# Performance work log

Measured on AMD Instinct MI355X. Metric: run time of the kernel, lower is better.

Reference implementation:

```python
import jax, jax.numpy as jnp
import numpy as np

T_ROIS = 200                       # TRAIN_ROIS_PER_IMAGE
POS_MAX = int(200 * 0.33)          # 66 max positives
R_RATIO = 1.0 / 0.33               # negative:positive ratio constant
MASK_SIZE = 28
BBOX_STD = np.array([0.1, 0.1, 0.2, 0.2], dtype=np.float32)


def _pairwise_iou(b1, b2):
    # b1 [N,4], b2 [G,4] -> [N,G]
    y1 = jnp.maximum(b1[:, None, 0], b2[None, :, 0])
    x1 = jnp.maximum(b1[:, None, 1], b2[None, :, 1])
    y2 = jnp.minimum(b1[:, None, 2], b2[None, :, 2])
    x2 = jnp.minimum(b1[:, None, 3], b2[None, :, 3])
    inter = jnp.maximum(x2 - x1, 0.0) * jnp.maximum(y2 - y1, 0.0)
    a1 = (b1[:, 2] - b1[:, 0]) * (b1[:, 3] - b1[:, 1])
    a2 = (b2[:, 2] - b2[:, 0]) * (b2[:, 3] - b2[:, 1])
    union = a1[:, None] + a2[None, :] - inter
    return jnp.where(union > 0, inter / jnp.where(union > 0, union, 1.0), 0.0)


def _box_refinement(box, gt):
    h = box[:, 2] - box[:, 0]
    w = box[:, 3] - box[:, 1]
    cy = box[:, 0] + 0.5 * h
    cx = box[:, 1] + 0.5 * w
    gh = gt[:, 2] - gt[:, 0]
    gw = gt[:, 3] - gt[:, 1]
    gcy = gt[:, 0] + 0.5 * gh
    gcx = gt[:, 1] + 0.5 * gw
    return jnp.stack([(gcy - cy) / h, (gcx - cx) / w,
                      jnp.log(gh / h), jnp.log(gw / w)], axis=1)


def _crop_and_resize(images, boxes, size):
    # TF tf.image.crop_and_resize (bilinear, extrapolation 0), images [K,H,W], boxes [K,4]
    K, H, W = images.shape
    y1, x1, y2, x2 = boxes[:, 0], boxes[:, 1], boxes[:, 2], boxes[:, 3]
    i = jnp.arange(size, dtype=images.dtype)
    ys = y1[:, None] * (H - 1) + i[None, :] * ((y2 - y1) * (H - 1) / (size - 1))[:, None]  # [K,S]
    xs = x1[:, None] * (W - 1) + i[None, :] * ((x2 - x1) * (W - 1) / (size - 1))[:, None]
    y0 = jnp.floor(ys)
    x0 = jnp.floor(xs)
    wy = (ys - y0)[:, :, None]   # [K,S,1]
    wx = (xs - x0)[:, None, :]   # [K,1,S]
    y0i = jnp.clip(y0, 0, H - 1).astype(jnp.int32)
    y1i = jnp.clip(y0 + 1, 0, H - 1).astype(jnp.int32)
    x0i = jnp.clip(x0, 0, W - 1).astype(jnp.int32)
    x1i = jnp.clip(x0 + 1, 0, W - 1).astype(jnp.int32)
    kk = jnp.arange(K)[:, None, None]
    v00 = images[kk, y0i[:, :, None], x0i[:, None, :]]
    v01 = images[kk, y0i[:, :, None], x1i[:, None, :]]
    v10 = images[kk, y1i[:, :, None], x0i[:, None, :]]
    v11 = images[kk, y1i[:, :, None], x1i[:, None, :]]
    val = (v00 * (1 - wx) + v01 * wx) * (1 - wy) + (v10 * (1 - wx) + v11 * wx) * wy
    ok = ((ys >= 0) & (ys <= H - 1))[:, :, None] & ((xs >= 0) & (xs <= W - 1))[:, None, :]
    return jnp.where(ok, val, 0.0)


def _detection_targets(proposals, gt_class_ids, gt_boxes, gt_masks):
    # proposals [N,4] f32, gt_class_ids [G] int32, gt_boxes [G,4] f32, gt_masks [H,W,G] bool
    valid_prop = jnp.sum(jnp.abs(proposals), axis=1) > 0          # trim_zeros (as mask)
    valid_gt = jnp.sum(jnp.abs(gt_boxes), axis=1) > 0
    is_crowd = valid_gt & (gt_class_ids < 0)
    is_fg = valid_gt & (gt_class_ids > 0)
    iou = _pairwise_iou(proposals, gt_boxes)                       # [N,G]
    iou = jnp.where(valid_prop[:, None], iou, 0.0)
    crowd_max = jnp.max(jnp.where(is_crowd[None, :], iou, 0.0), axis=1)
    no_crowd = crowd_max < 1e-3
    roi_iou_max = jnp.max(jnp.where(is_fg[None, :], iou, 0.0), axis=1)
    pos_bool = (roi_iou_max >= 0.5) & valid_prop
    neg_bool = (roi_iou_max < 0.5) & no_crowd & valid_prop
    num_pos = jnp.minimum(jnp.sum(pos_bool), POS_MAX)
    num_neg_want = jnp.floor(R_RATIO * num_pos.astype(jnp.float32)).astype(jnp.int32) - num_pos
    num_neg = jnp.clip(jnp.minimum(num_neg_want, jnp.sum(neg_bool)), 0, T_ROIS - num_pos)
    # deterministic subsample: lowest-index positives/negatives first (stable argsort)
    pos_order = jnp.argsort(jnp.logical_not(pos_bool))
    neg_order = jnp.argsort(jnp.logical_not(neg_bool))
    j = jnp.arange(T_ROIS)
    is_p = j < num_pos
    is_n = (j >= num_pos) & (j < num_pos + num_neg)
    sel = jnp.where(is_p, pos_order[j], neg_order[jnp.maximum(j - num_pos, 0)])
    keep = (is_p | is_n).astype(proposals.dtype)
    rois = proposals[sel] * keep[:, None]                          # zero-padded tail
    assign = jnp.argmax(jnp.where(is_fg[None, :], iou, -1.0)[sel], axis=1)
    class_ids = jnp.where(is_p, gt_class_ids[assign], 0)
    dummy = jnp.array([0.0, 0.0, 1.0, 1.0], dtype=proposals.dtype)  # safe box for padded rows
    p_roi = jnp.where(is_p[:, None], rois, dummy)
    p_gt = jnp.where(is_p[:, None], gt_boxes[assign], dummy)
    deltas = _box_refinement(p_roi, p_gt) / jnp.asarray(BBOX_STD)
    deltas = deltas * is_p[:, None]
    # mask targets: only first POS_MAX slots can be positive
    masks_t = jnp.transpose(gt_masks.astype(proposals.dtype), (2, 0, 1))   # [G,H,W]
    roi_m = masks_t[assign[:POS_MAX]]                              # [66,H,W]
    m = _crop_and_resize(roi_m, p_roi[:POS_MAX], MASK_SIZE)
    m = jnp.round(m) * is_p[:POS_MAX, None, None]
    masks = jnp.pad(m, ((0, T_ROIS - POS_MAX), (0, 0), (0, 0)))
    return rois, class_ids, deltas, masks


def _rand_boxes(k, shape):
    yx1 = jax.random.uniform(k, shape + (2,)) * 0.7
    hw = jax.random.uniform(jax.random.fold_in(k, 1), shape + (2,)) * 0.28 + 0.02
    return jnp.stack([yx1[..., 0], yx1[..., 1],
                      yx1[..., 0] + hw[..., 0], yx1[..., 1] + hw[..., 1]], axis=-1)


def setup_inputs() -> dict:
    key = jax.random.key(0)
    ks = jax.random.split(key, 6)
    B, N, G, H, W = 2, 2000, 100, 512, 512
    proposals = _rand_boxes(ks[0], (B, N))
    proposals = proposals * (jnp.arange(N) < int(N * 0.9))[None, :, None]  # zero-padded tail
    gt_boxes = _rand_boxes(ks[1], (B, G))
    gt_valid = jnp.arange(G) < 80
    gt_boxes = gt_boxes * gt_valid[None, :, None]
    cls = jax.random.randint(ks[2], (B, G), 1, 81).astype(jnp.int32)
    crowd = jax.random.uniform(ks[3], (B, G)) < 0.05
    cls = jnp.where(crowd, -cls, cls)
    cls = jnp.where(gt_valid[None, :], cls, 0)
    gt_masks = jax.random.randint(ks[4], (B, H, W, G), 0, 2).astype(bool)
    return {"proposals": proposals, "gt_class_ids": cls,
            "gt_boxes": gt_boxes, "gt_masks": gt_masks}


def reference(proposals, gt_class_ids, gt_boxes, gt_masks):
    return jax.vmap(_detection_targets)(proposals, gt_class_ids, gt_boxes, gt_masks)
```

## Files before the change

kernel.cpp:

```cpp
#include <hip/hip_runtime.h>
#include <math.h>

#define NPROP 2000
#define NGT   100
#define HH    512
#define WW    512
#define TR    200
#define PMAX  66
#define MS    28
#define FLAGS_OFF 4096

__global__ __launch_bounds__(256) void k_flags(
    const float* __restrict__ props,
    const int*   __restrict__ gcls,
    const float* __restrict__ gbox,
    int* __restrict__ wsi)
{
    const int b = blockIdx.y;
    const int i = blockIdx.x * 256 + threadIdx.x;
    const float* P  = props + (size_t)b * NPROP * 4;
    const float* GB = gbox  + (size_t)b * NGT * 4;
    const int*   GC = gcls  + (size_t)b * NGT;

    __shared__ float s_gb[NGT][4];
    __shared__ float s_garea[NGT];
    __shared__ unsigned char s_fg[NGT], s_crowd[NGT];

    if (threadIdx.x < NGT) {
        int t = threadIdx.x;
        float g0 = GB[t*4+0], g1 = GB[t*4+1], g2 = GB[t*4+2], g3 = GB[t*4+3];
        s_gb[t][0]=g0; s_gb[t][1]=g1; s_gb[t][2]=g2; s_gb[t][3]=g3;
        bool vg = (fabsf(g0)+fabsf(g1)+fabsf(g2)+fabsf(g3)) > 0.0f;
        int c = GC[t];
        s_fg[t]    = (unsigned char)(vg && (c > 0));
        s_crowd[t] = (unsigned char)(vg && (c < 0));
        s_garea[t] = __fmul_rn(__fsub_rn(g2,g0), __fsub_rn(g3,g1));
    }
    __syncthreads();

    if (i >= NPROP) return;
    float p0=P[i*4+0], p1=P[i*4+1], p2=P[i*4+2], p3=P[i*4+3];
    bool vp = (fabsf(p0)+fabsf(p1)+fabsf(p2)+fabsf(p3)) > 0.0f;
    float a1 = __fmul_rn(__fsub_rn(p2,p0), __fsub_rn(p3,p1));
    float crowd_max = 0.0f, fgmax = 0.0f;
    float best = -INFINITY; int arg = 0;
    for (int g = 0; g < NGT; ++g) {
        float y1 = fmaxf(p0, s_gb[g][0]);
        float x1 = fmaxf(p1, s_gb[g][1]);
        float y2 = fminf(p2, s_gb[g][2]);
        float x2 = fminf(p3, s_gb[g][3]);
        float inter = __fmul_rn(fmaxf(__fsub_rn(x2,x1), 0.0f),
                                fmaxf(__fsub_rn(y2,y1), 0.0f));
        float un = __fsub_rn(__fadd_rn(a1, s_garea[g]), inter);
        float iou = (un > 0.0f) ? __fdiv_rn(inter, un) : 0.0f;
        if (!vp) iou = 0.0f;
        if (s_crowd[g]) crowd_max = fmaxf(crowd_max, iou);
        float v;
        if (s_fg[g]) { fgmax = fmaxf(fgmax, iou); v = iou; }
        else         { v = -1.0f; }
        if (v > best) { best = v; arg = g; }
    }
    int pos = (int)((fgmax >= 0.5f) && vp);
    int neg = (int)((fgmax < 0.5f) && (crowd_max < 0.001f) && vp);
    wsi[FLAGS_OFF + b*NPROP + i] = pos | (neg << 1) | (arg << 2);
}

__global__ __launch_bounds__(512) void k_pick(
    const float* __restrict__ props,
    const int*   __restrict__ gcls,
    const float* __restrict__ gbox,
    float* __restrict__ out,
    int* __restrict__ wsi)
{
    const int b = blockIdx.x;
    const int t = threadIdx.x;
    const float* P  = props + (size_t)b * NPROP * 4;
    const float* GB = gbox  + (size_t)b * NGT * 4;
    const int*   GC = gcls  + (size_t)b * NGT;
    const int*   F  = wsi + FLAGS_OFF + b * NPROP;

    __shared__ int s_selp[PMAX], s_seln[TR], s_selpg[PMAX];
    __shared__ int s_wp[8], s_wn[8];
    __shared__ int s_totp, s_totn, s_np, s_nn;

    int t4 = t * 4;
    int fl[4]; int cp = 0, cn = 0;
    #pragma unroll
    for (int e = 0; e < 4; ++e) {
        int i = t4 + e;
        fl[e] = (i < NPROP) ? F[i] : 0;
        cp += (fl[e] & 1); cn += ((fl[e] >> 1) & 1);
    }
    int ip = cp, inn = cn;
    int lane = t & 63;
    #pragma unroll
    for (int d = 1; d < 64; d <<= 1) {
        int vp2 = __shfl_up(ip, d);
        int vn2 = __shfl_up(inn, d);
        if (lane >= d) { ip += vp2; inn += vn2; }
    }
    if (lane == 63) { s_wp[t >> 6] = ip; s_wn[t >> 6] = inn; }
    __syncthreads();
    if (t == 0) {
        int ap = 0, an = 0;
        for (int w = 0; w < 8; ++w) {
            int tp = s_wp[w]; s_wp[w] = ap; ap += tp;
            int tn = s_wn[w]; s_wn[w] = an; an += tn;
        }
        s_totp = ap; s_totn = an;
    }
    __syncthreads();
    int ep = s_wp[t >> 6] + ip - cp;
    int en = s_wn[t >> 6] + inn - cn;
    #pragma unroll
    for (int e = 0; e < 4; ++e) {
        if (fl[e] & 1) { if (ep < PMAX) { s_selp[ep] = t4 + e; s_selpg[ep] = (fl[e] >> 2) & 127; } ep++; }
        if ((fl[e] >> 1) & 1) { if (en < TR) s_seln[en] = t4 + e; en++; }
    }
    __syncthreads();

    if (t == 0) {
        int np = min(s_totp, PMAX);
        const float R = (float)(1.0 / 0.33);
        int want = (int)floorf(__fmul_rn(R, (float)np)) - np;
        int nn = min(want, s_totn);
        nn = min(nn, TR - np);
        nn = max(nn, 0);
        s_np = np; s_nn = nn;
        wsi[b] = np;
    }
    __syncthreads();

    if (t < TR) {
        const int j = t;
        const int np = s_np, nn = s_nn;
        const bool isp  = j < np;
        const bool kept = j < np + nn;
        float r0=0, r1=0, r2=0, r3=0, cid=0, d0=0, d1=0, d2=0, d3=0;
        if (kept) {
            int sel = isp ? s_selp[j] : s_seln[j - np];
            r0 = P[sel*4+0]; r1 = P[sel*4+1]; r2 = P[sel*4+2]; r3 = P[sel*4+3];
            if (isp) {
                int g = s_selpg[j];
                cid = (float)GC[g];
                float gb0 = GB[g*4+0], gb1 = GB[g*4+1], gb2 = GB[g*4+2], gb3 = GB[g*4+3];
                float h  = __fsub_rn(r2, r0), w = __fsub_rn(r3, r1);
                float cy = __fadd_rn(r0, __fmul_rn(0.5f, h));
                float cx = __fadd_rn(r1, __fmul_rn(0.5f, w));
                float gh  = __fsub_rn(gb2, gb0);
                float gw  = __fsub_rn(gb3, gb1);
                float gcy = __fadd_rn(gb0, __fmul_rn(0.5f, gh));
                float gcx = __fadd_rn(gb1, __fmul_rn(0.5f, gw));
                d0 = __fdiv_rn(__fdiv_rn(__fsub_rn(gcy, cy), h), 0.1f);
                d1 = __fdiv_rn(__fdiv_rn(__fsub_rn(gcx, cx), w), 0.1f);
                d2 = __fdiv_rn(logf(__fdiv_rn(gh, h)), 0.2f);
                d3 = __fdiv_rn(logf(__fdiv_rn(gw, w)), 0.2f);
                if (j < PMAX) {
                    wsi[2 + b*PMAX + j] = g;
                    float* wsf = (float*)(wsi + 2 + 2*PMAX);
                    wsf[(b*PMAX + j)*4 + 0] = r0;
                    wsf[(b*PMAX + j)*4 + 1] = r1;
                    wsf[(b*PMAX + j)*4 + 2] = r2;
                    wsf[(b*PMAX + j)*4 + 3] = r3;
                }
            }
        }
        out[(size_t)b*TR*4 + j*4 + 0] = r0;
        out[(size_t)b*TR*4 + j*4 + 1] = r1;
        out[(size_t)b*TR*4 + j*4 + 2] = r2;
        out[(size_t)b*TR*4 + j*4 + 3] = r3;
        out[1600 + (size_t)b*TR + j] = cid;
        out[2000 + (size_t)b*TR*4 + j*4 + 0] = d0;
        out[2000 + (size_t)b*TR*4 + j*4 + 1] = d1;
        out[2000 + (size_t)b*TR*4 + j*4 + 2] = d2;
        out[2000 + (size_t)b*TR*4 + j*4 + 3] = d3;
    }
}

__global__ __launch_bounds__(256) void k_masks(
    const int* __restrict__ gmask,
    const int* __restrict__ wsi,
    float* __restrict__ out)
{
    const int bid = blockIdx.x;
    const int b = bid / TR, j = bid % TR;
    float* mout = out + 3600 + (size_t)b*TR*MS*MS + (size_t)j*MS*MS;
    const int np = wsi[b];
    if (j >= np) {
        for (int p = threadIdx.x; p < MS*MS; p += 256) mout[p] = 0.0f;
        return;
    }
    const int g = wsi[2 + b*PMAX + j];
    const float* wsf = (const float*)(wsi + 2 + 2*PMAX);
    const float y1 = wsf[(b*PMAX + j)*4 + 0];
    const float x1 = wsf[(b*PMAX + j)*4 + 1];
    const float y2 = wsf[(b*PMAX + j)*4 + 2];
    const float x2 = wsf[(b*PMAX + j)*4 + 3];

    const float sy = __fdiv_rn(__fmul_rn(__fsub_rn(y2, y1), 511.0f), 27.0f);
    const float sx = __fdiv_rn(__fmul_rn(__fsub_rn(x2, x1), 511.0f), 27.0f);
    const float by = __fmul_rn(y1, 511.0f);
    const float bx = __fmul_rn(x1, 511.0f);
    const int* GM = gmask + (size_t)b * HH * WW * NGT + g;

    for (int p = threadIdx.x; p < MS*MS; p += 256) {
        int iy = p / MS, ix = p % MS;
        float ys = __fadd_rn(by, __fmul_rn((float)iy, sy));
        float xs = __fadd_rn(bx, __fmul_rn((float)ix, sx));
        float y0f = floorf(ys), x0f = floorf(xs);
        float wy = __fsub_rn(ys, y0f);
        float wx = __fsub_rn(xs, x0f);
        int y0i = (int)fminf(fmaxf(y0f, 0.0f), 511.0f);
        int y1i = (int)fminf(fmaxf(__fadd_rn(y0f, 1.0f), 0.0f), 511.0f);
        int x0i = (int)fminf(fmaxf(x0f, 0.0f), 511.0f);
        int x1i = (int)fminf(fmaxf(__fadd_rn(x0f, 1.0f), 0.0f), 511.0f);
        float v00 = (float)GM[((size_t)y0i * WW + x0i) * NGT];
        float v01 = (float)GM[((size_t)y0i * WW + x1i) * NGT];
        float v10 = (float)GM[((size_t)y1i * WW + x0i) * NGT];
        float v11 = (float)GM[((size_t)y1i * WW + x1i) * NGT];
        float omwx = __fsub_rn(1.0f, wx), omwy = __fsub_rn(1.0f, wy);
        float top = __fadd_rn(__fmul_rn(v00, omwx), __fmul_rn(v01, wx));
        float bot = __fadd_rn(__fmul_rn(v10, omwx), __fmul_rn(v11, wx));
        float val = __fadd_rn(__fmul_rn(top, omwy), __fmul_rn(bot, wy));
        bool ok = (ys >= 0.0f) && (ys <= 511.0f) && (xs >= 0.0f) && (xs <= 511.0f);
        val = ok ? val : 0.0f;
        mout[p] = rintf(val);
    }
}

extern "C" void kernel_launch(void* const* d_in, const int* in_sizes, int n_in,
                              void* d_out, int out_size, void* d_ws, size_t ws_size,
                              hipStream_t stream) {
    const float* props = (const float*)d_in[0];
    const int*   gcls  = (const int*)  d_in[1];
    const float* gbox  = (const float*)d_in[2];
    const int*   gmask = (const int*)  d_in[3];
    float* out = (float*)d_out;
    int* wsi = (int*)d_ws;

    dim3 gA(8, 2);
    k_flags<<<gA, 256, 0, stream>>>(props, gcls, gbox, wsi);
    k_pick<<<2, 512, 0, stream>>>(props, gcls, gbox, out, wsi);
    k_masks<<<2 * TR, 256, 0, stream>>>(gmask, wsi, out);
}
```

Before: 276.5 us.

## Fuse pick and mask kernels via per-row bitmask selection; split IoU across thread pairs

The flags kernel now gives each proposal to two threads, each scanning half the GT boxes, and merges the results with shuffles. It also writes per-block positive and negative bitmasks built with shared atomics. The separate single-block pick kernel is removed. Each of the 400 row blocks now locates its own proposal by walking the bitmask words with popcount and recomputes the sample counts, then goes straight on to the mask crop. This drops one kernel launch and the low-parallelism 2-block prefix-scan stage, at the cost of redundant selection work in every block and a serial bit walk on one thread.

Result: faster. 271.0 us (-2.0%).

```diff
diff --git a/kernel.cpp b/kernel.cpp
--- a/kernel.cpp
+++ b/kernel.cpp
@@ -9,6 +9,7 @@
 #define PMAX  66
 #define MS    28
 #define FLAGS_OFF 4096
+#define BITS_OFF  8192
 
 __global__ __launch_bounds__(256) void k_flags(
     const float* __restrict__ props,
@@ -17,7 +18,11 @@
     int* __restrict__ wsi)
 {
     const int b = blockIdx.y;
-    const int i = blockIdx.x * 256 + threadIdx.x;
+    const int t = threadIdx.x;
+    const int half = t & 1;
+    const int pairLocal = t >> 1;
+    const int pairId = blockIdx.x * 128 + pairLocal;
+    const bool act = pairId < NPROP;
     const float* P  = props + (size_t)b * NPROP * 4;
     const float* GB = gbox  + (size_t)b * NGT * 4;
     const int*   GC = gcls  + (size_t)b * NGT;
@@ -25,9 +30,10 @@
     __shared__ float s_gb[NGT][4];
     __shared__ float s_garea[NGT];
     __shared__ unsigned char s_fg[NGT], s_crowd[NGT];
-
-    if (threadIdx.x < NGT) {
-        int t = threadIdx.x;
+    __shared__ unsigned s_pw[4], s_nw[4];
+
+    if (t < 4) { s_pw[t] = 0u; s_nw[t] = 0u; }
+    if (t < NGT) {
         float g0 = GB[t*4+0], g1 = GB[t*4+1], g2 = GB[t*4+2], g3 = GB[t*4+3];
         s_gb[t][0]=g0; s_gb[t][1]=g1; s_gb[t][2]=g2; s_gb[t][3]=g3;
         bool vg = (fabsf(g0)+fabsf(g1)+fabsf(g2)+fabsf(g3)) > 0.0f;
@@ -38,13 +44,14 @@
     }
     __syncthreads();
 
-    if (i >= NPROP) return;
-    float p0=P[i*4+0], p1=P[i*4+1], p2=P[i*4+2], p3=P[i*4+3];
+    float p0=0.f, p1=0.f, p2=0.f, p3=0.f;
+    if (act) { p0=P[pairId*4+0]; p1=P[pairId*4+1]; p2=P[pairId*4+2]; p3=P[pairId*4+3]; }
     bool vp = (fabsf(p0)+fabsf(p1)+fabsf(p2)+fabsf(p3)) > 0.0f;
     float a1 = __fmul_rn(__fsub_rn(p2,p0), __fsub_rn(p3,p1));
     float crowd_max = 0.0f, fgmax = 0.0f;
-    float best = -INFINITY; int arg = 0;
-    for (int g = 0; g < NGT; ++g) {
+    float best = -INFINITY; int arg = half * 50;
+    const int g0i = half * 50;
+    for (int g = g0i; g < g0i + 50; ++g) {
         float y1 = fmaxf(p0, s_gb[g][0]);
         float x1 = fmaxf(p1, s_gb[g][1]);
         float y2 = fminf(p2, s_gb[g][2]);
@@ -60,88 +67,93 @@
         else         { v = -1.0f; }
         if (v > best) { best = v; arg = g; }
     }
+    float o;
+    o = __shfl_xor(fgmax, 1);     fgmax = fmaxf(fgmax, o);
+    o = __shfl_xor(crowd_max, 1); crowd_max = fmaxf(crowd_max, o);
+    float ob = __shfl_xor(best, 1); int oa = __shfl_xor(arg, 1);
+    float v_lo = half ? ob : best;  int a_lo = half ? oa : arg;
+    float v_hi = half ? best : ob;  int a_hi = half ? arg : oa;
+    int argf = (v_hi > v_lo) ? a_hi : a_lo;
     int pos = (int)((fgmax >= 0.5f) && vp);
     int neg = (int)((fgmax < 0.5f) && (crowd_max < 0.001f) && vp);
-    wsi[FLAGS_OFF + b*NPROP + i] = pos | (neg << 1) | (arg << 2);
+
+    if (act && half == 0) {
+        wsi[FLAGS_OFF + b*NPROP + pairId] = pos | (neg << 1) | (argf << 2);
+        unsigned bit = 1u << (pairLocal & 31);
+        int widx = pairLocal >> 5;
+        if (pos) atomicOr(&s_pw[widx], bit);
+        if (neg) atomicOr(&s_nw[widx], bit);
+    }
+    __syncthreads();
+    if (t < 4) {
+        unsigned* BW = (unsigned*)(wsi + BITS_OFF + b*128);
+        int w = blockIdx.x * 4 + t;
+        BW[w]      = s_pw[t];
+        BW[64 + w] = s_nw[t];
+    }
 }
 
-__global__ __launch_bounds__(512) void k_pick(
+__global__ __launch_bounds__(256) void k_rows(
     const float* __restrict__ props,
     const int*   __restrict__ gcls,
     const float* __restrict__ gbox,
-    float* __restrict__ out,
-    int* __restrict__ wsi)
+    const int*   __restrict__ gmask,
+    const int*   __restrict__ wsi,
+    float* __restrict__ out)
 {
-    const int b = blockIdx.x;
+    const int bid = blockIdx.x;
+    const int b = bid / TR, j = bid % TR;
     const int t = threadIdx.x;
+    const int lane = t & 63, wave = t >> 6;
     const float* P  = props + (size_t)b * NPROP * 4;
     const float* GB = gbox  + (size_t)b * NGT * 4;
     const int*   GC = gcls  + (size_t)b * NGT;
-    const int*   F  = wsi + FLAGS_OFF + b * NPROP;
-
-    __shared__ int s_selp[PMAX], s_seln[TR], s_selpg[PMAX];
-    __shared__ int s_wp[8], s_wn[8];
-    __shared__ int s_totp, s_totn, s_np, s_nn;
-
-    int t4 = t * 4;
-    int fl[4]; int cp = 0, cn = 0;
-    #pragma unroll
-    for (int e = 0; e < 4; ++e) {
-        int i = t4 + e;
-        fl[e] = (i < NPROP) ? F[i] : 0;
-        cp += (fl[e] & 1); cn += ((fl[e] >> 1) & 1);
-    }
-    int ip = cp, inn = cn;
-    int lane = t & 63;
-    #pragma unroll
-    for (int d = 1; d < 64; d <<= 1) {
-        int vp2 = __shfl_up(ip, d);
-        int vn2 = __shfl_up(inn, d);
-        if (lane >= d) { ip += vp2; inn += vn2; }
-    }
-    if (lane == 63) { s_wp[t >> 6] = ip; s_wn[t >> 6] = inn; }
-    __syncthreads();
+    const unsigned* BW = (const unsigned*)(wsi + BITS_OFF + b*128);
+
+    __shared__ unsigned s_w[2][63];
+    __shared__ int s_tot[2];
+    __shared__ int s_np, s_g;
+    __shared__ float s_r[4];
+
+    if (wave < 2) {
+        unsigned w = (lane < 63) ? BW[wave*64 + lane] : 0u;
+        if (lane < 63) s_w[wave][lane] = w;
+        int c = __popc(w);
+        #pragma unroll
+        for (int d = 1; d < 64; d <<= 1) c += __shfl_xor(c, d);
+        if (lane == 0) s_tot[wave] = c;
+    }
+    __syncthreads();
+
     if (t == 0) {
-        int ap = 0, an = 0;
-        for (int w = 0; w < 8; ++w) {
-            int tp = s_wp[w]; s_wp[w] = ap; ap += tp;
-            int tn = s_wn[w]; s_wn[w] = an; an += tn;
-        }
-        s_totp = ap; s_totn = an;
-    }
-    __syncthreads();
-    int ep = s_wp[t >> 6] + ip - cp;
-    int en = s_wn[t >> 6] + inn - cn;
-    #pragma unroll
-    for (int e = 0; e < 4; ++e) {
-        if (fl[e] & 1) { if (ep < PMAX) { s_selp[ep] = t4 + e; s_selpg[ep] = (fl[e] >> 2) & 127; } ep++; }
-        if ((fl[e] >> 1) & 1) { if (en < TR) s_seln[en] = t4 + e; en++; }
-    }
-    __syncthreads();
-
-    if (t == 0) {
-        int np = min(s_totp, PMAX);
+        int totp = s_tot[0], totn = s_tot[1];
+        int np = min(totp, PMAX);
         const float R = (float)(1.0 / 0.33);
         int want = (int)floorf(__fmul_rn(R, (float)np)) - np;
-        int nn = min(want, s_totn);
-        nn = min(nn, TR - np);
-        nn = max(nn, 0);
-        s_np = np; s_nn = nn;
-        wsi[b] = np;
-    }
-    __syncthreads();
-
-    if (t < TR) {
-        const int j = t;
-        const int np = s_np, nn = s_nn;
+        int nn = min(want, totn); nn = min(nn, TR - np); nn = max(nn, 0);
+        s_np = np;
         const bool isp  = j < np;
         const bool kept = j < np + nn;
         float r0=0, r1=0, r2=0, r3=0, cid=0, d0=0, d1=0, d2=0, d3=0;
+        int g = 0;
         if (kept) {
-            int sel = isp ? s_selp[j] : s_seln[j - np];
+            int list = isp ? 0 : 1;
+            int r = isp ? j : j - np;
+            int sel = 0;
+            for (int w = 0; w < 63; ++w) {
+                unsigned word = s_w[list][w];
+                int c = __popc(word);
+                if (r < c) {
+                    unsigned x = word;
+                    for (int k = 0; k < r; ++k) x &= x - 1;
+                    sel = w*32 + (__ffs(x) - 1);
+                    break;
+                }
+                r -= c;
+            }
             r0 = P[sel*4+0]; r1 = P[sel*4+1]; r2 = P[sel*4+2]; r3 = P[sel*4+3];
             if (isp) {
-                int g = s_selpg[j];
+                g = (wsi[FLAGS_OFF + b*NPROP + sel] >> 2) & 127;
                 cid = (float)GC[g];
                 float gb0 = GB[g*4+0], gb1 = GB[g*4+1], gb2 = GB[g*4+2], gb3 = GB[g*4+3];
                 float h  = __fsub_rn(r2, r0), w = __fsub_rn(r3, r1);
@@ -155,16 +167,9 @@
                 d1 = __fdiv_rn(__fdiv_rn(__fsub_rn(gcx, cx), w), 0.1f);
                 d2 = __fdiv_rn(logf(__fdiv_rn(gh, h)), 0.2f);
                 d3 = __fdiv_rn(logf(__fdiv_rn(gw, w)), 0.2f);
-                if (j < PMAX) {
-                    wsi[2 + b*PMAX + j] = g;
-                    float* wsf = (float*)(wsi + 2 + 2*PMAX);
-                    wsf[(b*PMAX + j)*4 + 0] = r0;
-                    wsf[(b*PMAX + j)*4 + 1] = r1;
-                    wsf[(b*PMAX + j)*4 + 2] = r2;
-                    wsf[(b*PMAX + j)*4 + 3] = r3;
-                }
             }
         }
+        s_g = g; s_r[0]=r0; s_r[1]=r1; s_r[2]=r2; s_r[3]=r3;
         out[(size_t)b*TR*4 + j*4 + 0] = r0;
         out[(size_t)b*TR*4 + j*4 + 1] = r1;
         out[(size_t)b*TR*4 + j*4 + 2] = r2;
@@ -175,35 +180,21 @@
         out[2000 + (size_t)b*TR*4 + j*4 + 2] = d2;
         out[2000 + (size_t)b*TR*4 + j*4 + 3] = d3;
     }
-}
-
-__global__ __launch_bounds__(256) void k_masks(
-    const int* __restrict__ gmask,
-    const int* __restrict__ wsi,
-    float* __restrict__ out)
-{
-    const int bid = blockIdx.x;
-    const int b = bid / TR, j = bid % TR;
+    __syncthreads();
+
     float* mout = out + 3600 + (size_t)b*TR*MS*MS + (size_t)j*MS*MS;
-    const int np = wsi[b];
-    if (j >= np) {
-        for (int p = threadIdx.x; p < MS*MS; p += 256) mout[p] = 0.0f;
+    if (j >= s_np) {
+        for (int p = t; p < MS*MS; p += 256) mout[p] = 0.0f;
         return;
     }
-    const int g = wsi[2 + b*PMAX + j];
-    const float* wsf = (const float*)(wsi + 2 + 2*PMAX);
-    const float y1 = wsf[(b*PMAX + j)*4 + 0];
-    const float x1 = wsf[(b*PMAX + j)*4 + 1];
-    const float y2 = wsf[(b*PMAX + j)*4 + 2];
-    const float x2 = wsf[(b*PMAX + j)*4 + 3];
-
+    const float y1 = s_r[0], x1 = s_r[1], y2 = s_r[2], x2 = s_r[3];
     const float sy = __fdiv_rn(__fmul_rn(__fsub_rn(y2, y1), 511.0f), 27.0f);
     const float sx = __fdiv_rn(__fmul_rn(__fsub_rn(x2, x1), 511.0f), 27.0f);
     const float by = __fmul_rn(y1, 511.0f);
     const float bx = __fmul_rn(x1, 511.0f);
-    const int* GM = gmask + (size_t)b * HH * WW * NGT + g;
-
-    for (int p = threadIdx.x; p < MS*MS; p += 256) {
+    const int* GM = gmask + (size_t)b * HH * WW * NGT + s_g;
+
+    for (int p = t; p < MS*MS; p += 256) {
         int iy = p / MS, ix = p % MS;
         float ys = __fadd_rn(by, __fmul_rn((float)iy, sy));
         float xs = __fadd_rn(bx, __fmul_rn((float)ix, sx));
@@ -238,8 +229,7 @@
     float* out = (float*)d_out;
     int* wsi = (int*)d_ws;
 
-    dim3 gA(8, 2);
+    dim3 gA(16, 2);
     k_flags<<<gA, 256, 0, stream>>>(props, gcls, gbox, wsi);
-    k_pick<<<2, 512, 0, stream>>>(props, gcls, gbox, out, wsi);
-    k_masks<<<2 * TR, 256, 0, stream>>>(gmask, wsi, out);
+    k_rows<<<2 * TR, 256, 0, stream>>>(props, gcls, gbox, gmask, wsi, out);
 }
```
